# Optimization experiments

Hardware: AMD Instinct MI355X
Metric: run time of the kernel (lower is better)

## Reference

```python
import jax, jax.numpy as jnp
import numpy as np

KERNEL_MUL = 2.0
KERNEL_NUM = 5


def _mmd(source, target):
    n = source.shape[0]
    m = target.shape[0]
    total = jnp.concatenate([source, target], axis=0)  # [n+m, d]
    sq = jnp.sum(total * total, axis=1)  # [n+m]
    l2 = sq[:, None] + sq[None, :] - 2.0 * (total @ total.T)  # [n+m, n+m]
    l2 = jnp.maximum(l2, 0.0)
    n_samples = n + m
    bandwidth = jnp.sum(l2) / (n_samples * n_samples - n_samples)
    bandwidth = bandwidth / (KERNEL_MUL ** (KERNEL_NUM // 2))
    # sum of KERNEL_NUM Gaussian kernels with geometric bandwidths
    kernels = sum(jnp.exp(-l2 / (bandwidth * KERNEL_MUL ** i)) for i in range(KERNEL_NUM))
    b = n  # batch_size = n, as in the torch code
    xx = jnp.sum(kernels[:b, :b]) / (n * n)
    yy = jnp.sum(kernels[b:, b:]) / (m * m)
    xy = jnp.sum(kernels[:b, b:]) / (n * m)
    yx = jnp.sum(kernels[b:, :b]) / (m * n)
    return xx + yy - xy - yx


def setup_inputs() -> dict:
    key = jax.random.key(0)
    k1, k2 = jax.random.split(key)
    source = jax.random.normal(k1, (4096, 256), dtype=jnp.float32)
    target = jax.random.normal(k2, (4096, 256), dtype=jnp.float32)
    return {"source": source, "target": target}


def reference(source, target):
    return _mmd(source, target)
```

## Files before the change

### kernel.cpp

```cpp
#include <hip/hip_runtime.h>
#include <hip/hip_bf16.h>

#define WS_D_COLSUM 0
#define WS_D_NEGG   256
#define WS_D_ACC    257
#define WS_ACC_SLOTS 32
#define WS_SQ_OFF   4096
#define WS_G_OFF    36864

#define NROW 8192
#define HALF 4096
#define DIM  256
#define TILE 128
#define NB   64
#define KC   32
#define NC   (DIM / KC)
#define BUFE (TILE * KC)

typedef short  short8 __attribute__((ext_vector_type(8)));
typedef float  f32x4  __attribute__((ext_vector_type(4)));
typedef unsigned short us4 __attribute__((ext_vector_type(4)));

static __device__ __forceinline__ unsigned short f2bfbits(float f) {
    __hip_bfloat16 h = __float2bfloat16(f);
    return *reinterpret_cast<unsigned short*>(&h);
}
static __device__ __forceinline__ float bfbits2f(unsigned short u) {
    return __uint_as_float(((unsigned int)u) << 16);
}
static __device__ __forceinline__ void gl_lds16(const void* g, void* l) {
    __builtin_amdgcn_global_load_lds(
        (const __attribute__((address_space(1))) void*)g,
        (__attribute__((address_space(3))) void*)l, 16, 0, 0);
}

__global__ __launch_bounds__(256) void k_prep(const float* __restrict__ src,
                                              const float* __restrict__ tgt,
                                              unsigned short* __restrict__ G,
                                              float* __restrict__ sq,
                                              double* __restrict__ colsum) {
    __shared__ float cs_lds[4 * 256];
    int t = threadIdx.x, wid = t >> 6, lane = t & 63;
    int r0 = blockIdx.x * 64;
    int c4 = lane * 4;

    float cs0 = 0.f, cs1 = 0.f, cs2 = 0.f, cs3 = 0.f;
    for (int i = 0; i < 16; ++i) {
        int row = r0 + wid + i * 4;
        const float* base = (row < HALF) ? (src + (size_t)row * DIM)
                                         : (tgt + (size_t)(row - HALF) * DIM);
        float4 v = *(const float4*)(base + c4);
        unsigned short u0 = f2bfbits(v.x), u1 = f2bfbits(v.y),
                       u2 = f2bfbits(v.z), u3 = f2bfbits(v.w);
        us4 uu = {u0, u1, u2, u3};
        *(us4*)(G + (size_t)row * DIM + c4) = uu;
        float r0f = bfbits2f(u0), r1f = bfbits2f(u1),
              r2f = bfbits2f(u2), r3f = bfbits2f(u3);
        cs0 += r0f; cs1 += r1f; cs2 += r2f; cs3 += r3f;
        float s = r0f * r0f + r1f * r1f + r2f * r2f + r3f * r3f;
        #pragma unroll
        for (int off = 32; off; off >>= 1) s += __shfl_down(s, off);
        if (lane == 0) sq[row] = s;
    }
    cs_lds[wid * 256 + c4 + 0] = cs0;
    cs_lds[wid * 256 + c4 + 1] = cs1;
    cs_lds[wid * 256 + c4 + 2] = cs2;
    cs_lds[wid * 256 + c4 + 3] = cs3;
    __syncthreads();
    double s = (double)cs_lds[t] + (double)cs_lds[256 + t] +
               (double)cs_lds[512 + t] + (double)cs_lds[768 + t];
    atomicAdd(&colsum[t], s);
}

__global__ __launch_bounds__(256) void k_bw(const float* __restrict__ sq,
                                            double* __restrict__ wsd) {
    __shared__ double red[256];
    __shared__ double red2[256];
    int t = threadIdx.x;
    double s = 0.0;
    for (int i = t; i < NROW; i += 256) s += (double)sq[i];
    double c = wsd[WS_D_COLSUM + t];
    red[t]  = s;
    red2[t] = c * c;
    __syncthreads();
    for (int off = 128; off; off >>= 1) {
        if (t < off) { red[t] += red[t + off]; red2[t] += red2[t + off]; }
        __syncthreads();
    }
    if (t == 0) {
        const double N = (double)NROW;
        double sum_l2 = 2.0 * N * red[0] - 2.0 * red2[0];
        double bw = sum_l2 / (N * N - N);
        bw = bw / 4.0;
        wsd[WS_D_NEGG] = -1.4426950408889634 / (16.0 * bw);
    }
}

__global__ __launch_bounds__(256, 3) void k_mmd(const unsigned short* __restrict__ G,
                                                const float* __restrict__ sq,
                                                const double* __restrict__ wsd,
                                                double* __restrict__ acc_slots) {
    __shared__ unsigned short As[3 * BUFE];
    __shared__ unsigned short Bs[3 * BUFE];
    __shared__ double wsum[4];

    int bi = 0, rem = blockIdx.x;
    while (rem >= NB - bi) { rem -= NB - bi; ++bi; }
    int bj = bi + rem;

    int t = threadIdx.x, wid = t >> 6, lane = t & 63;
    int wr = wid >> 1, wc = wid & 1;
    int rl = lane & 15, klane = lane >> 4;

    const unsigned short* Abase = G + (size_t)bi * TILE * DIM;
    const unsigned short* Bbase = G + (size_t)bj * TILE * DIM;

    int lr0 = wid * 32 + (lane >> 2);
    int slog0 = (lane & 3) ^ ((lr0 >> 1) & 3);
    int lr1 = lr0 + 16;
    int slog1 = (lane & 3) ^ ((lr1 >> 1) & 3);
    size_t ga0 = (size_t)lr0 * DIM + slog0 * 8;
    size_t ga1 = (size_t)lr1 * DIM + slog1 * 8;
    int ld0 = (wid * 32) * KC;
    int ld1 = (wid * 32 + 16) * KC;

    int aoff[4], boff[4];
    #pragma unroll
    for (int f = 0; f < 4; ++f) {
        int ra = wr * 64 + f * 16 + rl;
        aoff[f] = ra * KC + ((klane ^ ((ra >> 1) & 3)) * 8);
        int rb = wc * 64 + f * 16 + rl;
        boff[f] = rb * KC + ((klane ^ ((rb >> 1) & 3)) * 8);
    }

    const f32x4 zero4 = {0.f, 0.f, 0.f, 0.f};
    f32x4 acc[4][4];
    #pragma unroll
    for (int i = 0; i < 4; ++i)
        #pragma unroll
        for (int j = 0; j < 4; ++j) acc[i][j] = zero4;

    #define STAGE(kc, b)                                                     \
        do {                                                                 \
            gl_lds16(Abase + ga0 + (kc) * KC, &As[(b) * BUFE + ld0]);        \
            gl_lds16(Bbase + ga0 + (kc) * KC, &Bs[(b) * BUFE + ld0]);        \
            gl_lds16(Abase + ga1 + (kc) * KC, &As[(b) * BUFE + ld1]);        \
            gl_lds16(Bbase + ga1 + (kc) * KC, &Bs[(b) * BUFE + ld1]);        \
        } while (0)

    STAGE(0, 0);
    STAGE(1, 1);

    #pragma unroll
    for (int kc = 0; kc < NC; ++kc) {
        if (kc < NC - 1) { asm volatile("s_waitcnt vmcnt(4)" ::: "memory"); }
        else             { asm volatile("s_waitcnt vmcnt(0)" ::: "memory"); }
        __builtin_amdgcn_s_barrier();
        __builtin_amdgcn_sched_barrier(0);
        if (kc + 2 < NC) STAGE(kc + 2, (kc + 2) % 3);

        const unsigned short* Ab = &As[(kc % 3) * BUFE];
        const unsigned short* Bb = &Bs[(kc % 3) * BUFE];
        short8 af[4], bfv[4];
        #pragma unroll
        for (int f = 0; f < 4; ++f) {
            af[f]  = *(const short8*)&Ab[aoff[f]];
            bfv[f] = *(const short8*)&Bb[boff[f]];
        }
        #pragma unroll
        for (int i = 0; i < 4; ++i)
            #pragma unroll
            for (int j = 0; j < 4; ++j)
                acc[i][j] = __builtin_amdgcn_mfma_f32_16x16x32_bf16(af[i], bfv[j], acc[i][j], 0, 0, 0);
    }
    #undef STAGE

    int gi0 = bi * TILE + wr * 64;
    int gj0 = bj * TILE + wc * 64;
    float ng2 = (float)wsd[WS_D_NEGG];
    int rgrp = lane >> 4;

    float sqb4[4];
    #pragma unroll
    for (int j = 0; j < 4; ++j) sqb4[j] = sq[gj0 + j * 16 + rl];

    float tsum = 0.f;
    #pragma unroll
    for (int i = 0; i < 4; ++i) {
        float sqa4[4];
        #pragma unroll
        for (int rr = 0; rr < 4; ++rr) sqa4[rr] = sq[gi0 + i * 16 + rgrp * 4 + rr];
        #pragma unroll
        for (int j = 0; j < 4; ++j) {
            #pragma unroll
            for (int rr = 0; rr < 4; ++rr) {
                float l2 = fmaxf(sqa4[rr] + sqb4[j] - 2.0f * acc[i][j][rr], 0.f);
                float e   = exp2f(l2 * ng2);
                float e2  = e * e;
                float e4  = e2 * e2;
                float e8  = e4 * e4;
                float e16 = e8 * e8;
                tsum += e + e2 + e4 + e8 + e16;
            }
        }
    }

    float w = ((bi < 32) == (bj < 32)) ? 1.f : -1.f;
    if (bi != bj) w *= 2.f;
    double dsum = (double)tsum * (double)w;

    #pragma unroll
    for (int off = 32; off; off >>= 1) dsum += __shfl_down(dsum, off);
    if (lane == 0) wsum[wid] = dsum;
    __syncthreads();
    if (t == 0)
        atomicAdd(&acc_slots[blockIdx.x & (WS_ACC_SLOTS - 1)],
                  wsum[0] + wsum[1] + wsum[2] + wsum[3]);
}

__global__ void k_final(const double* __restrict__ wsd, float* __restrict__ out) {
    double s = 0.0;
    for (int i = 0; i < WS_ACC_SLOTS; ++i) s += wsd[WS_D_ACC + i];
    out[0] = (float)(s / ((double)HALF * (double)HALF));
}

extern "C" void kernel_launch(void* const* d_in, const int* in_sizes, int n_in,
                              void* d_out, int out_size, void* d_ws, size_t ws_size,
                              hipStream_t stream) {
    const float* src = (const float*)d_in[0];
    const float* tgt = (const float*)d_in[1];
    float* out = (float*)d_out;

    double* wsd       = (double*)d_ws;
    float* sq         = (float*)((char*)d_ws + WS_SQ_OFF);
    unsigned short* G = (unsigned short*)((char*)d_ws + WS_G_OFF);

    hipMemsetAsync(d_ws, 0, 4096, stream);

    k_prep<<<128, 256, 0, stream>>>(src, tgt, G, sq, &wsd[WS_D_COLSUM]);
    k_bw<<<1, 256, 0, stream>>>(sq, wsd);

    int nblocks = NB * (NB + 1) / 2;
    k_mmd<<<nblocks, 256, 0, stream>>>(G, sq, wsd, &wsd[WS_D_ACC]);

    k_final<<<1, 1, 0, stream>>>(wsd, out);
}
```

Measured before the change: 73.21 us.

## Prepack bf16 Gram operands in MFMA fragment order and drop LDS staging

The prep kernel now writes the bf16 matrix in a per-64-row tile layout that matches MFMA fragment order, so each lane can load its operands with contiguous 16-byte global loads. The main kernel no longer stages through LDS: each wavefront independently computes one 64x64 upper-triangle tile pair, double-buffering register fragments from global/L2. Blocks are swizzled across the grid and each wave does its own atomic. This removes LDS traffic and barriers, but operand reuse across waves now depends on the cache, and global traffic roughly doubles because tiles are smaller.

```diff
diff --git a/kernel.cpp b/kernel.cpp
--- a/kernel.cpp
+++ b/kernel.cpp
@@ -11,11 +11,11 @@
 #define NROW 8192
 #define HALF 4096
 #define DIM  256
-#define TILE 128
-#define NB   64
-#define KC   32
-#define NC   (DIM / KC)
-#define BUFE (TILE * KC)
+#define TT   64
+#define NT   128
+#define NPAIR (NT * (NT + 1) / 2)
+#define NBLK  (NPAIR / 4)
+#define TILE_US (8 * 4 * 512)
 
 typedef short  short8 __attribute__((ext_vector_type(8)));
 typedef float  f32x4  __attribute__((ext_vector_type(4)));
@@ -28,21 +28,18 @@
 static __device__ __forceinline__ float bfbits2f(unsigned short u) {
     return __uint_as_float(((unsigned int)u) << 16);
 }
-static __device__ __forceinline__ void gl_lds16(const void* g, void* l) {
-    __builtin_amdgcn_global_load_lds(
-        (const __attribute__((address_space(1))) void*)g,
-        (__attribute__((address_space(3))) void*)l, 16, 0, 0);
-}
 
 __global__ __launch_bounds__(256) void k_prep(const float* __restrict__ src,
                                               const float* __restrict__ tgt,
-                                              unsigned short* __restrict__ G,
+                                              unsigned short* __restrict__ G2,
                                               float* __restrict__ sq,
                                               double* __restrict__ colsum) {
     __shared__ float cs_lds[4 * 256];
     int t = threadIdx.x, wid = t >> 6, lane = t & 63;
     int r0 = blockIdx.x * 64;
     int c4 = lane * 4;
+    int lanepart = (lane >> 3) * 2048 + ((lane >> 1) & 3) * 128 + (lane & 1) * 4;
+    size_t tilebase = (size_t)blockIdx.x * TILE_US;
 
     float cs0 = 0.f, cs1 = 0.f, cs2 = 0.f, cs3 = 0.f;
     for (int i = 0; i < 16; ++i) {
@@ -53,7 +50,8 @@
         unsigned short u0 = f2bfbits(v.x), u1 = f2bfbits(v.y),
                        u2 = f2bfbits(v.z), u3 = f2bfbits(v.w);
         us4 uu = {u0, u1, u2, u3};
-        *(us4*)(G + (size_t)row * DIM + c4) = uu;
+        int fr = (row >> 4) & 3, rl = row & 15;
+        *(us4*)(G2 + tilebase + fr * 512 + rl * 8 + lanepart) = uu;
         float r0f = bfbits2f(u0), r1f = bfbits2f(u1),
               r2f = bfbits2f(u2), r3f = bfbits2f(u3);
         cs0 += r0f; cs1 += r1f; cs2 += r2f; cs3 += r3f;
@@ -96,42 +94,22 @@
     }
 }
 
-__global__ __launch_bounds__(256, 3) void k_mmd(const unsigned short* __restrict__ G,
+__global__ __launch_bounds__(256, 3) void k_mmd(const unsigned short* __restrict__ G2,
                                                 const float* __restrict__ sq,
                                                 const double* __restrict__ wsd,
                                                 double* __restrict__ acc_slots) {
-    __shared__ unsigned short As[3 * BUFE];
-    __shared__ unsigned short Bs[3 * BUFE];
-    __shared__ double wsum[4];
-
-    int bi = 0, rem = blockIdx.x;
-    while (rem >= NB - bi) { rem -= NB - bi; ++bi; }
-    int bj = bi + rem;
-
-    int t = threadIdx.x, wid = t >> 6, lane = t & 63;
-    int wr = wid >> 1, wc = wid & 1;
-    int rl = lane & 15, klane = lane >> 4;
-
-    const unsigned short* Abase = G + (size_t)bi * TILE * DIM;
-    const unsigned short* Bbase = G + (size_t)bj * TILE * DIM;
-
-    int lr0 = wid * 32 + (lane >> 2);
-    int slog0 = (lane & 3) ^ ((lr0 >> 1) & 3);
-    int lr1 = lr0 + 16;
-    int slog1 = (lane & 3) ^ ((lr1 >> 1) & 3);
-    size_t ga0 = (size_t)lr0 * DIM + slog0 * 8;
-    size_t ga1 = (size_t)lr1 * DIM + slog1 * 8;
-    int ld0 = (wid * 32) * KC;
-    int ld1 = (wid * 32 + 16) * KC;
-
-    int aoff[4], boff[4];
-    #pragma unroll
-    for (int f = 0; f < 4; ++f) {
-        int ra = wr * 64 + f * 16 + rl;
-        aoff[f] = ra * KC + ((klane ^ ((ra >> 1) & 3)) * 8);
-        int rb = wc * 64 + f * 16 + rl;
-        boff[f] = rb * KC + ((klane ^ ((rb >> 1) & 3)) * 8);
-    }
+    int bid = blockIdx.x;
+    int swz = (bid & 7) * (NBLK / 8) + (bid >> 3);
+
+    int wid = threadIdx.x >> 6, lane = threadIdx.x & 63;
+    int p = swz * 4 + wid;
+    int ti = 0, rem = p;
+    while (rem >= NT - ti) { rem -= NT - ti; ++ti; }
+    int tj = ti + rem;
+
+    const unsigned short* Ab = G2 + (size_t)ti * TILE_US;
+    const unsigned short* Bb = G2 + (size_t)tj * TILE_US;
+    int lo = lane * 8;
 
     const f32x4 zero4 = {0.f, 0.f, 0.f, 0.f};
     f32x4 acc[4][4];
@@ -140,49 +118,45 @@
         #pragma unroll
         for (int j = 0; j < 4; ++j) acc[i][j] = zero4;
 
-    #define STAGE(kc, b)                                                     \
-        do {                                                                 \
-            gl_lds16(Abase + ga0 + (kc) * KC, &As[(b) * BUFE + ld0]);        \
-            gl_lds16(Bbase + ga0 + (kc) * KC, &Bs[(b) * BUFE + ld0]);        \
-            gl_lds16(Abase + ga1 + (kc) * KC, &As[(b) * BUFE + ld1]);        \
-            gl_lds16(Bbase + ga1 + (kc) * KC, &Bs[(b) * BUFE + ld1]);        \
+    short8 a0[4], b0[4], a1[4], b1[4];
+
+    #define LOADSET(A, B, kc)                                            \
+        do {                                                             \
+            _Pragma("unroll")                                            \
+            for (int f = 0; f < 4; ++f) {                                \
+                A[f] = *(const short8*)&Ab[((kc) * 4 + f) * 512 + lo];   \
+                B[f] = *(const short8*)&Bb[((kc) * 4 + f) * 512 + lo];   \
+            }                                                            \
         } while (0)
-
-    STAGE(0, 0);
-    STAGE(1, 1);
-
-    #pragma unroll
-    for (int kc = 0; kc < NC; ++kc) {
-        if (kc < NC - 1) { asm volatile("s_waitcnt vmcnt(4)" ::: "memory"); }
-        else             { asm volatile("s_waitcnt vmcnt(0)" ::: "memory"); }
-        __builtin_amdgcn_s_barrier();
-        __builtin_amdgcn_sched_barrier(0);
-        if (kc + 2 < NC) STAGE(kc + 2, (kc + 2) % 3);
-
-        const unsigned short* Ab = &As[(kc % 3) * BUFE];
-        const unsigned short* Bb = &Bs[(kc % 3) * BUFE];
-        short8 af[4], bfv[4];
-        #pragma unroll
-        for (int f = 0; f < 4; ++f) {
-            af[f]  = *(const short8*)&Ab[aoff[f]];
-            bfv[f] = *(const short8*)&Bb[boff[f]];
-        }
-        #pragma unroll
-        for (int i = 0; i < 4; ++i)
-            #pragma unroll
-            for (int j = 0; j < 4; ++j)
-                acc[i][j] = __builtin_amdgcn_mfma_f32_16x16x32_bf16(af[i], bfv[j], acc[i][j], 0, 0, 0);
-    }
-    #undef STAGE
-
-    int gi0 = bi * TILE + wr * 64;
-    int gj0 = bj * TILE + wc * 64;
+    #define MFMASET(A, B)                                                \
+        do {                                                             \
+            _Pragma("unroll")                                            \
+            for (int i = 0; i < 4; ++i)                                  \
+                _Pragma("unroll")                                        \
+                for (int j = 0; j < 4; ++j)                              \
+                    acc[i][j] = __builtin_amdgcn_mfma_f32_16x16x32_bf16( \
+                        A[i], B[j], acc[i][j], 0, 0, 0);                 \
+        } while (0)
+
+    LOADSET(a0, b0, 0);
+    #pragma unroll
+    for (int k2 = 0; k2 < 4; ++k2) {
+        LOADSET(a1, b1, 2 * k2 + 1);
+        MFMASET(a0, b0);
+        if (k2 < 3) LOADSET(a0, b0, 2 * k2 + 2);
+        MFMASET(a1, b1);
+    }
+    #undef LOADSET
+    #undef MFMASET
+
+    int gi0 = ti * TT;
+    int gj0 = tj * TT;
     float ng2 = (float)wsd[WS_D_NEGG];
-    int rgrp = lane >> 4;
+    int rl16 = lane & 15, rgrp = lane >> 4;
 
     float sqb4[4];
     #pragma unroll
-    for (int j = 0; j < 4; ++j) sqb4[j] = sq[gj0 + j * 16 + rl];
+    for (int j = 0; j < 4; ++j) sqb4[j] = sq[gj0 + j * 16 + rl16];
 
     float tsum = 0.f;
     #pragma unroll
@@ -205,17 +179,14 @@
         }
     }
 
-    float w = ((bi < 32) == (bj < 32)) ? 1.f : -1.f;
-    if (bi != bj) w *= 2.f;
+    float w = ((ti < NT / 2) == (tj < NT / 2)) ? 1.f : -1.f;
+    if (ti != tj) w *= 2.f;
     double dsum = (double)tsum * (double)w;
 
     #pragma unroll
     for (int off = 32; off; off >>= 1) dsum += __shfl_down(dsum, off);
-    if (lane == 0) wsum[wid] = dsum;
-    __syncthreads();
-    if (t == 0)
-        atomicAdd(&acc_slots[blockIdx.x & (WS_ACC_SLOTS - 1)],
-                  wsum[0] + wsum[1] + wsum[2] + wsum[3]);
+    if (lane == 0)
+        atomicAdd(&acc_slots[p & (WS_ACC_SLOTS - 1)], dsum);
 }
 
 __global__ void k_final(const double* __restrict__ wsd, float* __restrict__ out) {
@@ -231,17 +202,16 @@
     const float* tgt = (const float*)d_in[1];
     float* out = (float*)d_out;
 
-    double* wsd       = (double*)d_ws;
-    float* sq         = (float*)((char*)d_ws + WS_SQ_OFF);
-    unsigned short* G = (unsigned short*)((char*)d_ws + WS_G_OFF);
+    double* wsd        = (double*)d_ws;
+    float* sq          = (float*)((char*)d_ws + WS_SQ_OFF);
+    unsigned short* G2 = (unsigned short*)((char*)d_ws + WS_G_OFF);
 
     hipMemsetAsync(d_ws, 0, 4096, stream);
 
-    k_prep<<<128, 256, 0, stream>>>(src, tgt, G, sq, &wsd[WS_D_COLSUM]);
+    k_prep<<<NROW / 64, 256, 0, stream>>>(src, tgt, G2, sq, &wsd[WS_D_COLSUM]);
     k_bw<<<1, 256, 0, stream>>>(sq, wsd);
 
-    int nblocks = NB * (NB + 1) / 2;
-    k_mmd<<<nblocks, 256, 0, stream>>>(G, sq, wsd, &wsd[WS_D_ACC]);
+    k_mmd<<<NBLK, 256, 0, stream>>>(G2, sq, wsd, &wsd[WS_D_ACC]);
 
     k_final<<<1, 1, 0, stream>>>(wsd, out);
 }
```

New measurement: 94.93 us. 29.7% more time.

## Fuse bandwidth and final reduction into last-block epilogues, double-buffer LDS

Applied to the files above, without the earlier changes.

Removes the separate bandwidth and final-sum kernels. The last block to finish (found with an atomic ticket counter) now does those reductions, which saves two launches and their serialization gaps. The GEMM staging drops from a triple to a double LDS buffer, waiting for all loads each iteration. This frees LDS but weakens load/compute overlap. The exponent epilogue folds the bandwidth scale into the squared norms and uses packed float2 math to cut VALU ops.

```diff
diff --git a/kernel.cpp b/kernel.cpp
--- a/kernel.cpp
+++ b/kernel.cpp
@@ -3,22 +3,26 @@
 
 #define WS_D_COLSUM 0
 #define WS_D_NEGG   256
-#define WS_D_ACC    257
-#define WS_ACC_SLOTS 32
-#define WS_SQ_OFF   4096
-#define WS_G_OFF    36864
+#define WS_D_SQSUM  257
+#define WS_D_SLOT   258
+#define WS_SLOTS    64
+#define WS_TICK_OFF 4112
+#define WS_SQ_OFF   4608
+#define WS_G_OFF    40960
 
 #define NROW 8192
 #define HALF 4096
 #define DIM  256
 #define TILE 128
 #define NB   64
+#define NBLK (NB * (NB + 1) / 2)
 #define KC   32
 #define NC   (DIM / KC)
 #define BUFE (TILE * KC)
 
 typedef short  short8 __attribute__((ext_vector_type(8)));
 typedef float  f32x4  __attribute__((ext_vector_type(4)));
+typedef float  f32x2  __attribute__((ext_vector_type(2)));
 typedef unsigned short us4 __attribute__((ext_vector_type(4)));
 
 static __device__ __forceinline__ unsigned short f2bfbits(float f) {
@@ -38,13 +42,19 @@
                                               const float* __restrict__ tgt,
                                               unsigned short* __restrict__ G,
                                               float* __restrict__ sq,
-                                              double* __restrict__ colsum) {
+                                              double* __restrict__ wsd,
+                                              int* __restrict__ tick) {
     __shared__ float cs_lds[4 * 256];
+    __shared__ double sq_lds[4];
+    __shared__ double red2[256];
+    __shared__ int is_last;
+
     int t = threadIdx.x, wid = t >> 6, lane = t & 63;
     int r0 = blockIdx.x * 64;
     int c4 = lane * 4;
 
     float cs0 = 0.f, cs1 = 0.f, cs2 = 0.f, cs3 = 0.f;
+    double wsq = 0.0;
     for (int i = 0; i < 16; ++i) {
         int row = r0 + wid + i * 4;
         const float* base = (row < HALF) ? (src + (size_t)row * DIM)
@@ -60,36 +70,36 @@
         float s = r0f * r0f + r1f * r1f + r2f * r2f + r3f * r3f;
         #pragma unroll
         for (int off = 32; off; off >>= 1) s += __shfl_down(s, off);
-        if (lane == 0) sq[row] = s;
+        if (lane == 0) { sq[row] = s; wsq += (double)s; }
     }
     cs_lds[wid * 256 + c4 + 0] = cs0;
     cs_lds[wid * 256 + c4 + 1] = cs1;
     cs_lds[wid * 256 + c4 + 2] = cs2;
     cs_lds[wid * 256 + c4 + 3] = cs3;
+    if (lane == 0) sq_lds[wid] = wsq;
     __syncthreads();
     double s = (double)cs_lds[t] + (double)cs_lds[256 + t] +
                (double)cs_lds[512 + t] + (double)cs_lds[768 + t];
-    atomicAdd(&colsum[t], s);
-}
-
-__global__ __launch_bounds__(256) void k_bw(const float* __restrict__ sq,
-                                            double* __restrict__ wsd) {
-    __shared__ double red[256];
-    __shared__ double red2[256];
-    int t = threadIdx.x;
-    double s = 0.0;
-    for (int i = t; i < NROW; i += 256) s += (double)sq[i];
-    double c = wsd[WS_D_COLSUM + t];
-    red[t]  = s;
+    atomicAdd(&wsd[WS_D_COLSUM + t], s);
+    if (t == 0)
+        atomicAdd(&wsd[WS_D_SQSUM], sq_lds[0] + sq_lds[1] + sq_lds[2] + sq_lds[3]);
+    __threadfence();
+    __syncthreads();
+    if (t == 0) is_last = (atomicAdd(tick, 1) == (int)gridDim.x - 1);
+    __syncthreads();
+    if (!is_last) return;
+
+    double c = atomicAdd(&wsd[WS_D_COLSUM + t], 0.0);
     red2[t] = c * c;
     __syncthreads();
     for (int off = 128; off; off >>= 1) {
-        if (t < off) { red[t] += red[t + off]; red2[t] += red2[t + off]; }
+        if (t < off) red2[t] += red2[t + off];
         __syncthreads();
     }
     if (t == 0) {
+        double S = atomicAdd(&wsd[WS_D_SQSUM], 0.0);
         const double N = (double)NROW;
-        double sum_l2 = 2.0 * N * red[0] - 2.0 * red2[0];
+        double sum_l2 = 2.0 * N * S - 2.0 * red2[0];
         double bw = sum_l2 / (N * N - N);
         bw = bw / 4.0;
         wsd[WS_D_NEGG] = -1.4426950408889634 / (16.0 * bw);
@@ -99,10 +109,13 @@
 __global__ __launch_bounds__(256, 3) void k_mmd(const unsigned short* __restrict__ G,
                                                 const float* __restrict__ sq,
                                                 const double* __restrict__ wsd,
-                                                double* __restrict__ acc_slots) {
-    __shared__ unsigned short As[3 * BUFE];
-    __shared__ unsigned short Bs[3 * BUFE];
+                                                double* __restrict__ slots,
+                                                float* __restrict__ out,
+                                                int* __restrict__ tick) {
+    __shared__ unsigned short As[2 * BUFE];
+    __shared__ unsigned short Bs[2 * BUFE];
     __shared__ double wsum[4];
+    __shared__ int is_last;
 
     int bi = 0, rem = blockIdx.x;
     while (rem >= NB - bi) { rem -= NB - bi; ++bi; }
@@ -149,18 +162,15 @@
         } while (0)
 
     STAGE(0, 0);
-    STAGE(1, 1);
-
     #pragma unroll
     for (int kc = 0; kc < NC; ++kc) {
-        if (kc < NC - 1) { asm volatile("s_waitcnt vmcnt(4)" ::: "memory"); }
-        else             { asm volatile("s_waitcnt vmcnt(0)" ::: "memory"); }
+        asm volatile("s_waitcnt vmcnt(0)" ::: "memory");
         __builtin_amdgcn_s_barrier();
         __builtin_amdgcn_sched_barrier(0);
-        if (kc + 2 < NC) STAGE(kc + 2, (kc + 2) % 3);
-
-        const unsigned short* Ab = &As[(kc % 3) * BUFE];
-        const unsigned short* Bb = &Bs[(kc % 3) * BUFE];
+        if (kc + 1 < NC) STAGE(kc + 1, (kc + 1) & 1);
+
+        const unsigned short* Ab = &As[(kc & 1) * BUFE];
+        const unsigned short* Bb = &Bs[(kc & 1) * BUFE];
         short8 af[4], bfv[4];
         #pragma unroll
         for (int f = 0; f < 4; ++f) {
@@ -171,39 +181,47 @@
         for (int i = 0; i < 4; ++i)
             #pragma unroll
             for (int j = 0; j < 4; ++j)
-                acc[i][j] = __builtin_amdgcn_mfma_f32_16x16x32_bf16(af[i], bfv[j], acc[i][j], 0, 0, 0);
+                acc[i][j] = __builtin_amdgcn_mfma_f32_16x16x32_bf16(
+                    af[i], bfv[j], acc[i][j], 0, 0, 0);
     }
     #undef STAGE
 
     int gi0 = bi * TILE + wr * 64;
     int gj0 = bj * TILE + wc * 64;
     float ng2 = (float)wsd[WS_D_NEGG];
+    float m2g = -2.0f * ng2;
+    f32x2 m2g2 = {m2g, m2g};
     int rgrp = lane >> 4;
 
     float sqb4[4];
     #pragma unroll
-    for (int j = 0; j < 4; ++j) sqb4[j] = sq[gj0 + j * 16 + rl];
-
-    float tsum = 0.f;
+    for (int j = 0; j < 4; ++j) sqb4[j] = sq[gj0 + j * 16 + rl] * ng2;
+
+    f32x2 tsv = {0.f, 0.f};
     #pragma unroll
     for (int i = 0; i < 4; ++i) {
-        float sqa4[4];
-        #pragma unroll
-        for (int rr = 0; rr < 4; ++rr) sqa4[rr] = sq[gi0 + i * 16 + rgrp * 4 + rr];
+        int base = gi0 + i * 16 + rgrp * 4;
+        f32x2 sa01 = {sq[base + 0] * ng2, sq[base + 1] * ng2};
+        f32x2 sa23 = {sq[base + 2] * ng2, sq[base + 3] * ng2};
         #pragma unroll
         for (int j = 0; j < 4; ++j) {
-            #pragma unroll
-            for (int rr = 0; rr < 4; ++rr) {
-                float l2 = fmaxf(sqa4[rr] + sqb4[j] - 2.0f * acc[i][j][rr], 0.f);
-                float e   = exp2f(l2 * ng2);
-                float e2  = e * e;
-                float e4  = e2 * e2;
-                float e8  = e4 * e4;
-                float e16 = e8 * e8;
-                tsum += e + e2 + e4 + e8 + e16;
-            }
+            f32x2 sb = {sqb4[j], sqb4[j]};
+            f32x2 x01 = {acc[i][j][0], acc[i][j][1]};
+            f32x2 x23 = {acc[i][j][2], acc[i][j][3]};
+            x01 = x01 * m2g2 + (sa01 + sb);
+            x23 = x23 * m2g2 + (sa23 + sb);
+            f32x2 e01, e23;
+            e01.x = exp2f(x01.x); e01.y = exp2f(x01.y);
+            e23.x = exp2f(x23.x); e23.y = exp2f(x23.y);
+            f32x2 p01 = e01 * e01, q01 = p01 * p01,
+                  r01 = q01 * q01, s01 = r01 * r01;
+            f32x2 p23 = e23 * e23, q23 = p23 * p23,
+                  r23 = q23 * q23, s23 = r23 * r23;
+            tsv += ((e01 + p01) + (q01 + r01)) + s01;
+            tsv += ((e23 + p23) + (q23 + r23)) + s23;
         }
     }
+    float tsum = tsv.x + tsv.y;
 
     float w = ((bi < 32) == (bj < 32)) ? 1.f : -1.f;
     if (bi != bj) w *= 2.f;
@@ -214,14 +232,21 @@
     if (lane == 0) wsum[wid] = dsum;
     __syncthreads();
     if (t == 0)
-        atomicAdd(&acc_slots[blockIdx.x & (WS_ACC_SLOTS - 1)],
+        atomicAdd(&slots[blockIdx.x & (WS_SLOTS - 1)],
                   wsum[0] + wsum[1] + wsum[2] + wsum[3]);
-}
-
-__global__ void k_final(const double* __restrict__ wsd, float* __restrict__ out) {
-    double s = 0.0;
-    for (int i = 0; i < WS_ACC_SLOTS; ++i) s += wsd[WS_D_ACC + i];
-    out[0] = (float)(s / ((double)HALF * (double)HALF));
+    __threadfence();
+    __syncthreads();
+    if (t == 0) is_last = (atomicAdd(tick, 1) == NBLK - 1);
+    __syncthreads();
+    if (!is_last) return;
+
+    if (wid == 0) {
+        double v = atomicAdd(&slots[lane], 0.0);
+        #pragma unroll
+        for (int off = 32; off; off >>= 1) v += __shfl_down(v, off);
+        if (lane == 0)
+            out[0] = (float)(v / ((double)HALF * (double)HALF));
+    }
 }
 
 extern "C" void kernel_launch(void* const* d_in, const int* in_sizes, int n_in,
@@ -232,16 +257,12 @@
     float* out = (float*)d_out;
 
     double* wsd       = (double*)d_ws;
+    int* ticks        = (int*)((char*)d_ws + WS_TICK_OFF);
     float* sq         = (float*)((char*)d_ws + WS_SQ_OFF);
     unsigned short* G = (unsigned short*)((char*)d_ws + WS_G_OFF);
 
-    hipMemsetAsync(d_ws, 0, 4096, stream);
-
-    k_prep<<<128, 256, 0, stream>>>(src, tgt, G, sq, &wsd[WS_D_COLSUM]);
-    k_bw<<<1, 256, 0, stream>>>(sq, wsd);
-
-    int nblocks = NB * (NB + 1) / 2;
-    k_mmd<<<nblocks, 256, 0, stream>>>(G, sq, wsd, &wsd[WS_D_ACC]);
-
-    k_final<<<1, 1, 0, stream>>>(wsd, out);
-}
+    hipMemsetAsync(d_ws, 0, WS_SQ_OFF, stream);
+
+    k_prep<<<NROW / 64, 256, 0, stream>>>(src, tgt, G, sq, wsd, &ticks[0]);
+    k_mmd<<<NBLK, 256, 0, stream>>>(G, sq, wsd, &wsd[WS_D_SLOT], out, &ticks[1]);
+}
```

Result: slower. 180.9 us (+147.1%).

## Spread prep over more blocks with banked atomics and pack epilogue math

Applied to the files above, without the earlier changes.

The prep kernel now runs 512 blocks of 16 rows instead of 128 blocks of 64 rows. Its column-sum atomics are spread over 8 banks to reduce contention, and it also accumulates per-bank sums of squared norms. The MMD epilogue folds the bandwidth scale into the squared norms and uses packed 2-wide float math with an FMA, replacing the separate fmax/multiply. The final reduction uses 64 slots instead of 32. The banked layout enlarges the memset, and k_bw still recomputes the squared-norm sum itself, so the new SQSUM values go unused.

```diff
diff --git a/kernel.cpp b/kernel.cpp
--- a/kernel.cpp
+++ b/kernel.cpp
@@ -1,24 +1,28 @@
 #include <hip/hip_runtime.h>
 #include <hip/hip_bf16.h>
 
-#define WS_D_COLSUM 0
-#define WS_D_NEGG   256
-#define WS_D_ACC    257
-#define WS_ACC_SLOTS 32
-#define WS_SQ_OFF   4096
-#define WS_G_OFF    36864
+#define WS_D_COLSUM8 0
+#define WS_D_SQSUM8  2048
+#define WS_D_NEGG    2056
+#define WS_D_SLOT    2057
+#define WS_SLOTS     64
+#define WS_MEMSET_B  16968
+#define WS_SQ_OFF    17152
+#define WS_G_OFF     50176
 
 #define NROW 8192
 #define HALF 4096
 #define DIM  256
 #define TILE 128
 #define NB   64
+#define NBLK (NB * (NB + 1) / 2)
 #define KC   32
 #define NC   (DIM / KC)
 #define BUFE (TILE * KC)
 
 typedef short  short8 __attribute__((ext_vector_type(8)));
 typedef float  f32x4  __attribute__((ext_vector_type(4)));
+typedef float  f32x2  __attribute__((ext_vector_type(2)));
 typedef unsigned short us4 __attribute__((ext_vector_type(4)));
 
 static __device__ __forceinline__ unsigned short f2bfbits(float f) {
@@ -38,14 +42,18 @@
                                               const float* __restrict__ tgt,
                                               unsigned short* __restrict__ G,
                                               float* __restrict__ sq,
-                                              double* __restrict__ colsum) {
+                                              double* __restrict__ wsd) {
     __shared__ float cs_lds[4 * 256];
+    __shared__ double sq_lds[4];
+
     int t = threadIdx.x, wid = t >> 6, lane = t & 63;
-    int r0 = blockIdx.x * 64;
+    int r0 = blockIdx.x * 16;
     int c4 = lane * 4;
+    int bank = blockIdx.x & 7;
 
     float cs0 = 0.f, cs1 = 0.f, cs2 = 0.f, cs3 = 0.f;
-    for (int i = 0; i < 16; ++i) {
+    double wsq = 0.0;
+    for (int i = 0; i < 4; ++i) {
         int row = r0 + wid + i * 4;
         const float* base = (row < HALF) ? (src + (size_t)row * DIM)
                                          : (tgt + (size_t)(row - HALF) * DIM);
@@ -60,16 +68,20 @@
         float s = r0f * r0f + r1f * r1f + r2f * r2f + r3f * r3f;
         #pragma unroll
         for (int off = 32; off; off >>= 1) s += __shfl_down(s, off);
-        if (lane == 0) sq[row] = s;
+        if (lane == 0) { sq[row] = s; wsq += (double)s; }
     }
     cs_lds[wid * 256 + c4 + 0] = cs0;
     cs_lds[wid * 256 + c4 + 1] = cs1;
     cs_lds[wid * 256 + c4 + 2] = cs2;
     cs_lds[wid * 256 + c4 + 3] = cs3;
+    if (lane == 0) sq_lds[wid] = wsq;
     __syncthreads();
     double s = (double)cs_lds[t] + (double)cs_lds[256 + t] +
                (double)cs_lds[512 + t] + (double)cs_lds[768 + t];
-    atomicAdd(&colsum[t], s);
+    atomicAdd(&wsd[WS_D_COLSUM8 + bank * 256 + t], s);
+    if (t == 0)
+        atomicAdd(&wsd[WS_D_SQSUM8 + bank],
+                  sq_lds[0] + sq_lds[1] + sq_lds[2] + sq_lds[3]);
 }
 
 __global__ __launch_bounds__(256) void k_bw(const float* __restrict__ sq,
@@ -79,7 +91,9 @@
     int t = threadIdx.x;
     double s = 0.0;
     for (int i = t; i < NROW; i += 256) s += (double)sq[i];
-    double c = wsd[WS_D_COLSUM + t];
+    double c = 0.0;
+    #pragma unroll
+    for (int p = 0; p < 8; ++p) c += wsd[WS_D_COLSUM8 + p * 256 + t];
     red[t]  = s;
     red2[t] = c * c;
     __syncthreads();
@@ -99,7 +113,7 @@
 __global__ __launch_bounds__(256, 3) void k_mmd(const unsigned short* __restrict__ G,
                                                 const float* __restrict__ sq,
                                                 const double* __restrict__ wsd,
-                                                double* __restrict__ acc_slots) {
+                                                double* __restrict__ slots) {
     __shared__ unsigned short As[3 * BUFE];
     __shared__ unsigned short Bs[3 * BUFE];
     __shared__ double wsum[4];
@@ -171,39 +185,47 @@
         for (int i = 0; i < 4; ++i)
             #pragma unroll
             for (int j = 0; j < 4; ++j)
-                acc[i][j] = __builtin_amdgcn_mfma_f32_16x16x32_bf16(af[i], bfv[j], acc[i][j], 0, 0, 0);
+                acc[i][j] = __builtin_amdgcn_mfma_f32_16x16x32_bf16(
+                    af[i], bfv[j], acc[i][j], 0, 0, 0);
     }
     #undef STAGE
 
     int gi0 = bi * TILE + wr * 64;
     int gj0 = bj * TILE + wc * 64;
     float ng2 = (float)wsd[WS_D_NEGG];
+    float m2g = -2.0f * ng2;
+    f32x2 m2g2 = {m2g, m2g};
     int rgrp = lane >> 4;
 
     float sqb4[4];
     #pragma unroll
-    for (int j = 0; j < 4; ++j) sqb4[j] = sq[gj0 + j * 16 + rl];
-
-    float tsum = 0.f;
+    for (int j = 0; j < 4; ++j) sqb4[j] = sq[gj0 + j * 16 + rl] * ng2;
+
+    f32x2 tsv = {0.f, 0.f};
     #pragma unroll
     for (int i = 0; i < 4; ++i) {
-        float sqa4[4];
-        #pragma unroll
-        for (int rr = 0; rr < 4; ++rr) sqa4[rr] = sq[gi0 + i * 16 + rgrp * 4 + rr];
+        int base = gi0 + i * 16 + rgrp * 4;
+        f32x2 sa01 = {sq[base + 0] * ng2, sq[base + 1] * ng2};
+        f32x2 sa23 = {sq[base + 2] * ng2, sq[base + 3] * ng2};
         #pragma unroll
         for (int j = 0; j < 4; ++j) {
-            #pragma unroll
-            for (int rr = 0; rr < 4; ++rr) {
-                float l2 = fmaxf(sqa4[rr] + sqb4[j] - 2.0f * acc[i][j][rr], 0.f);
-                float e   = exp2f(l2 * ng2);
-                float e2  = e * e;
-                float e4  = e2 * e2;
-                float e8  = e4 * e4;
-                float e16 = e8 * e8;
-                tsum += e + e2 + e4 + e8 + e16;
-            }
+            f32x2 sb = {sqb4[j], sqb4[j]};
+            f32x2 x01 = {acc[i][j][0], acc[i][j][1]};
+            f32x2 x23 = {acc[i][j][2], acc[i][j][3]};
+            x01 = x01 * m2g2 + (sa01 + sb);
+            x23 = x23 * m2g2 + (sa23 + sb);
+            f32x2 e01, e23;
+            e01.x = exp2f(x01.x); e01.y = exp2f(x01.y);
+            e23.x = exp2f(x23.x); e23.y = exp2f(x23.y);
+            f32x2 p01 = e01 * e01, q01 = p01 * p01,
+                  r01 = q01 * q01, s01 = r01 * r01;
+            f32x2 p23 = e23 * e23, q23 = p23 * p23,
+                  r23 = q23 * q23, s23 = r23 * r23;
+            tsv += ((e01 + p01) + (q01 + r01)) + s01;
+            tsv += ((e23 + p23) + (q23 + r23)) + s23;
         }
     }
+    float tsum = tsv.x + tsv.y;
 
     float w = ((bi < 32) == (bj < 32)) ? 1.f : -1.f;
     if (bi != bj) w *= 2.f;
@@ -214,13 +236,13 @@
     if (lane == 0) wsum[wid] = dsum;
     __syncthreads();
     if (t == 0)
-        atomicAdd(&acc_slots[blockIdx.x & (WS_ACC_SLOTS - 1)],
+        atomicAdd(&slots[blockIdx.x & (WS_SLOTS - 1)],
                   wsum[0] + wsum[1] + wsum[2] + wsum[3]);
 }
 
 __global__ void k_final(const double* __restrict__ wsd, float* __restrict__ out) {
     double s = 0.0;
-    for (int i = 0; i < WS_ACC_SLOTS; ++i) s += wsd[WS_D_ACC + i];
+    for (int i = 0; i < WS_SLOTS; ++i) s += wsd[WS_D_SLOT + i];
     out[0] = (float)(s / ((double)HALF * (double)HALF));
 }
 
@@ -235,13 +257,10 @@
     float* sq         = (float*)((char*)d_ws + WS_SQ_OFF);
     unsigned short* G = (unsigned short*)((char*)d_ws + WS_G_OFF);
 
-    hipMemsetAsync(d_ws, 0, 4096, stream);
-
-    k_prep<<<128, 256, 0, stream>>>(src, tgt, G, sq, &wsd[WS_D_COLSUM]);
+    hipMemsetAsync(d_ws, 0, WS_MEMSET_B, stream);
+
+    k_prep<<<NROW / 16, 256, 0, stream>>>(src, tgt, G, sq, wsd);
     k_bw<<<1, 256, 0, stream>>>(sq, wsd);
-
-    int nblocks = NB * (NB + 1) / 2;
-    k_mmd<<<nblocks, 256, 0, stream>>>(G, sq, wsd, &wsd[WS_D_ACC]);
-
+    k_mmd<<<NBLK, 256, 0, stream>>>(G, sq, wsd, &wsd[WS_D_SLOT]);
     k_final<<<1, 1, 0, stream>>>(wsd, out);
 }
```

Result: faster. 65.46 us (-10.6%).
